# Optimization experiments

Hardware: AMD Instinct MI355X
Metric: run time of the kernel (lower is better)

The kernel has to match this reference:

```python
import jax, jax.numpy as jnp
import numpy as np

B, S, D = 4, 2048, 512
H, DH = 8, 64  # head_num, atten_dim
EPS = 1e-5


def setup_inputs() -> dict:
    key = jax.random.key(0)
    ks = jax.random.split(key, 24)
    sc_in = 1.0 / np.sqrt(D)
    sc_hid = 1.0 / np.sqrt(H * DH)
    inp = {}
    names = ["Q_data", "Q_time", "K_data", "K_time", "V_data", "V_time"]
    for i, n in enumerate(names):
        inp[n] = jax.random.normal(ks[i], (B, S, D), dtype=jnp.float32)
    # projection weights stored as [in, out]
    pnames = ["q_d", "q_t", "k_d", "k_t", "v_d", "v_t"]
    for i, p in enumerate(pnames):
        inp["W" + p] = jax.random.normal(ks[6 + 2 * i], (D, H * DH), dtype=jnp.float32) * sc_in
        inp["b" + p] = jax.random.normal(ks[7 + 2 * i], (H * DH,), dtype=jnp.float32) * 0.01
    inp["Wo"] = jax.random.normal(ks[18], (H * DH, D), dtype=jnp.float32) * sc_hid
    inp["bo"] = jax.random.normal(ks[19], (D,), dtype=jnp.float32) * 0.01
    inp["gamma"] = jnp.ones((D,), dtype=jnp.float32)
    inp["beta"] = jnp.zeros((D,), dtype=jnp.float32)
    return inp


def _proj(x, W, b):
    # [B,S,D] @ [D,H*DH] -> [B,S,H,DH]
    return (jnp.einsum('bsd,de->bse', x, W) + b).reshape(B, S, H, DH)


def reference(Q_data, Q_time, K_data, K_time, V_data, V_time,
              Wq_d, bq_d, Wq_t, bq_t, Wk_d, bk_d, Wk_t, bk_t,
              Wv_d, bv_d, Wv_t, bv_t, Wo, bo, gamma, beta):
    residual = Q_data
    qd = _proj(Q_data, Wq_d, bq_d)
    qt = _proj(Q_time, Wq_t, bq_t)
    kd = _proj(K_data, Wk_d, bk_d)
    kt = _proj(K_time, Wk_t, bk_t)
    vd = _proj(V_data, Wv_d, bv_d)
    vt = _proj(V_time, Wv_t, bv_t)
    scale = 1.0 / np.sqrt(DH)
    # combined dual-stream scores: [B,H,S,S]
    scores = (jnp.einsum('bshd,bthd->bhst', qd, kd)
              + jnp.einsum('bshd,bthd->bhst', qt, kt)) * scale
    attn = jax.nn.softmax(scores, axis=-1)
    # dual V context, summed: [B,S,H,DH]
    ctx = jnp.einsum('bhst,bthd->bshd', attn, vd + vt)
    ctx = ctx.reshape(B, S, H * DH)
    out = jnp.einsum('bse,ed->bsd', ctx, Wo) + bo
    x = out + residual
    mu = jnp.mean(x, axis=-1, keepdims=True)
    var = jnp.var(x, axis=-1, keepdims=True)
    return (x - mu) * jax.lax.rsqrt(var + EPS) * gamma + beta
```

## Files before the change

### kernel.cpp

```cpp
#include <hip/hip_runtime.h>
#include <hip/hip_bf16.h>

#define DEVI __device__ __forceinline__

typedef __attribute__((ext_vector_type(4))) float f32x4;
typedef __attribute__((ext_vector_type(8))) short s16x8;
typedef __bf16 bf16x8 __attribute__((ext_vector_type(8)));

static constexpr int B_ = 4, S_ = 2048, D_ = 512, H_ = 8;
static constexpr int BS = B_ * S_;
static constexpr float QSCALE = 0.125f * 1.4426950408889634f;

DEVI unsigned short f2bf(float x) {
  union { float f; unsigned int u; } v; v.f = x;
  unsigned int r = v.u + 0x7FFFu + ((v.u >> 16) & 1u);
  return (unsigned short)(r >> 16);
}

DEVI void gload16(const void* g, void* l) {
  __builtin_amdgcn_global_load_lds(
      (const __attribute__((address_space(1))) unsigned int*)g,
      (__attribute__((address_space(3))) unsigned int*)l, 16, 0, 0);
}

DEVI f32x4 mfma16(s16x8 a, s16x8 b, f32x4 c) {
  return __builtin_amdgcn_mfma_f32_16x16x32_bf16(
      __builtin_bit_cast(bf16x8, a), __builtin_bit_cast(bf16x8, b), c, 0, 0, 0);
}

__global__ void k_cvt_x(const float* __restrict__ x0, const float* __restrict__ x1,
                        const float* __restrict__ x2, const float* __restrict__ x3,
                        const float* __restrict__ x4, const float* __restrict__ x5,
                        unsigned short* __restrict__ xc) {
  const int p = blockIdx.y;
  const float* x = (p == 0) ? x0 : (p == 1) ? x1 : (p == 2) ? x2
                 : (p == 3) ? x3 : (p == 4) ? x4 : x5;
  const int i = (blockIdx.x * 256 + threadIdx.x) * 4;
  const float4 v = *(const float4*)(x + i);
  ushort4 o;
  o.x = f2bf(v.x); o.y = f2bf(v.y); o.z = f2bf(v.z); o.w = f2bf(v.w);
  *(ushort4*)(xc + (size_t)p * BS * D_ + i) = o;
}

__global__ void k_cvt_w(const float* __restrict__ w0, const float* __restrict__ w1,
                        const float* __restrict__ w2, const float* __restrict__ w3,
                        const float* __restrict__ w4, const float* __restrict__ w5,
                        const float* __restrict__ w6, unsigned short* __restrict__ wt) {
  const int p = blockIdx.y;
  const float* w = (p == 0) ? w0 : (p == 1) ? w1 : (p == 2) ? w2
                 : (p == 3) ? w3 : (p == 4) ? w4 : (p == 5) ? w5 : w6;
  __shared__ float t[32][33];
  const int tx = threadIdx.x, ty = threadIdx.y;
  const int tn = (blockIdx.x & 15) * 32, tk = (blockIdx.x >> 4) * 32;
#pragma unroll
  for (int i = 0; i < 4; ++i)
    t[ty + i * 8][tx] = w[(size_t)(tk + ty + i * 8) * 512 + tn + tx];
  __syncthreads();
#pragma unroll
  for (int i = 0; i < 4; ++i)
    wt[(size_t)p * 262144 + (size_t)(tn + ty + i * 8) * 512 + tk + tx] =
        f2bf(t[tx][ty + i * 8]);
}

__launch_bounds__(256, 2)
__global__ void k_proj(const unsigned short* __restrict__ Xc, const unsigned short* __restrict__ Wt,
                       const float* __restrict__ b0, const float* __restrict__ b1,
                       const float* __restrict__ b2, const float* __restrict__ b3,
                       const float* __restrict__ b4, const float* __restrict__ b5,
                       unsigned short* __restrict__ Qc, unsigned short* __restrict__ Kc,
                       unsigned short* __restrict__ Vt) {
  __shared__ unsigned short As[128 * 32], Bs[128 * 32];
  const int p = blockIdx.y;
  const int m0 = (blockIdx.x >> 2) * 128, n0 = (blockIdx.x & 3) * 128;
  const int tid = threadIdx.x, w = tid >> 6, lane = tid & 63;
  const int g = lane >> 4, cl = lane & 15;
  const int wm = (w >> 1) * 64, wn = (w & 1) * 64;
  f32x4 acc[4][4];
#pragma unroll
  for (int i = 0; i < 4; ++i)
#pragma unroll
    for (int j = 0; j < 4; ++j) { acc[i][j][0] = 0.f; acc[i][j][1] = 0.f; acc[i][j][2] = 0.f; acc[i][j][3] = 0.f; }

  const int npass = (p == 4) ? 2 : 1;
  for (int pass = 0; pass < npass; ++pass) {
    const int src = (p == 4) ? (4 + pass) : p;
    const unsigned short* A = Xc + (size_t)src * BS * 512;
    const unsigned short* Bw = Wt + (size_t)src * 262144;
    for (int k0 = 0; k0 < 512; k0 += 32) {
#pragma unroll
      for (int i = 0; i < 2; ++i) {
        const int c = i * 256 + tid;
        gload16(A + (size_t)(m0 + (c >> 2)) * 512 + k0 + (c & 3) * 8,
                (char*)As + (i * 256 + w * 64) * 16);
        gload16(Bw + (size_t)(n0 + (c >> 2)) * 512 + k0 + (c & 3) * 8,
                (char*)Bs + (i * 256 + w * 64) * 16);
      }
      __syncthreads();
      s16x8 af[4], bf[4];
#pragma unroll
      for (int t = 0; t < 4; ++t) {
        af[t] = *(const s16x8*)(As + (wm + t * 16 + cl) * 32 + g * 8);
        bf[t] = *(const s16x8*)(Bs + (wn + t * 16 + cl) * 32 + g * 8);
      }
#pragma unroll
      for (int mt = 0; mt < 4; ++mt)
#pragma unroll
        for (int nt = 0; nt < 4; ++nt)
          acc[mt][nt] = mfma16(af[mt], bf[nt], acc[mt][nt]);
      __syncthreads();
    }
  }
  const float scale = (p <= 1) ? QSCALE : 1.0f;
#pragma unroll
  for (int nt = 0; nt < 4; ++nt) {
    const int n = n0 + wn + nt * 16 + cl;
    float bias;
    if (p == 0) bias = b0[n]; else if (p == 1) bias = b1[n];
    else if (p == 2) bias = b2[n]; else if (p == 3) bias = b3[n];
    else bias = b4[n] + b5[n];
    const int h = n >> 6, dh = n & 63;
    if (p == 4) {
#pragma unroll
      for (int mt = 0; mt < 4; ++mt) {
        const int m = m0 + wm + mt * 16 + g * 4;
        const int bb = m >> 11, s = m & 2047;
        ushort4 o4;
        o4.x = f2bf(acc[mt][nt][0] + bias);
        o4.y = f2bf(acc[mt][nt][1] + bias);
        o4.z = f2bf(acc[mt][nt][2] + bias);
        o4.w = f2bf(acc[mt][nt][3] + bias);
        *(ushort4*)(&Vt[((size_t)(bb * 8 + h) * 64 + dh) * 2048 + s]) = o4;
      }
    } else {
#pragma unroll
      for (int mt = 0; mt < 4; ++mt)
#pragma unroll
        for (int r = 0; r < 4; ++r) {
          const int m = m0 + wm + mt * 16 + g * 4 + r;
          const int bb = m >> 11, s = m & 2047;
          const unsigned short o = f2bf((acc[mt][nt][r] + bias) * scale);
          if (p <= 1) {
            Qc[(((size_t)(bb * 8 + h) * 2048 + s) << 7) + dh + p * 64] = o;
          } else {
            const int dk = dh + (p - 2) * 64;
            Kc[(((size_t)(bb * 8 + h) * 2048 + s) << 7) + (dk ^ ((s & 7) << 3))] = o;
          }
        }
    }
  }
}

__launch_bounds__(256, 1)
__global__ void k_attn(const unsigned short* __restrict__ Qc, const unsigned short* __restrict__ Kc,
                       const unsigned short* __restrict__ Vt, unsigned short* __restrict__ Cx) {
  __shared__ unsigned short Ks[2][64 * 128];
  __shared__ unsigned short Ps[4][64 * 88];
  const int bid = blockIdx.x;
  const int xcd = bid & 7, idx = bid >> 3;
  const int bh = xcd | ((idx & 3) << 3);
  const int qblk = idx >> 2;
  const int tid = threadIdx.x, w = tid >> 6, lane = tid & 63;
  const int g = lane >> 4, cl = lane & 15;
  const unsigned short* Qb = Qc + (size_t)bh * S_ * 128;
  const unsigned short* Kb = Kc + (size_t)bh * S_ * 128;
  const unsigned short* Vb = Vt + (size_t)bh * 64 * S_;
  const int q0 = qblk * 256 + w * 64;

  s16x8 qf[4][4];
#pragma unroll
  for (int qb = 0; qb < 4; ++qb)
#pragma unroll
    for (int ks = 0; ks < 4; ++ks)
      qf[qb][ks] = *(const s16x8*)(Qb + (size_t)(q0 + qb * 16 + cl) * 128 + ks * 32 + g * 8);

  const f32x4 z4 = {0.f, 0.f, 0.f, 0.f};
  f32x4 ctx[4][5];
#pragma unroll
  for (int qb = 0; qb < 4; ++qb)
#pragma unroll
    for (int nt = 0; nt < 5; ++nt) ctx[qb][nt] = z4;

  const unsigned short* vrow[4];
#pragma unroll
  for (int nt = 0; nt < 4; ++nt) vrow[nt] = Vb + (size_t)(nt * 16 + cl) * 2048 + g * 8;

  const unsigned short* kptr[4];
#pragma unroll
  for (int i = 0; i < 4; ++i)
    kptr[i] = Kb + (size_t)((w * 4 + i) * 4 + (lane >> 4)) * 128 + (lane & 15) * 8;

  const short onev = (cl == 0) ? (short)0x3F80 : (short)0;
  const s16x8 vfo = {onev, onev, onev, onev, onev, onev, onev, onev};

  unsigned short* Pw = Ps[w];

#pragma unroll
  for (int i = 0; i < 4; ++i) {
    gload16(kptr[i], (char*)Ks[0] + (w * 4 + i) * 1024);
    kptr[i] += 64 * 128;
  }
  __syncthreads();

  const int NT = S_ / 64;
  for (int t = 0; t < NT; ++t) {
    const int b = t & 1;
    if (t + 1 < NT) {
#pragma unroll
      for (int i = 0; i < 4; ++i) {
        gload16(kptr[i], (char*)Ks[b ^ 1] + (w * 4 + i) * 1024);
        kptr[i] += 64 * 128;
      }
    }
    s16x8 vreg[2][4];
#pragma unroll
    for (int kk = 0; kk < 2; ++kk)
#pragma unroll
      for (int nt = 0; nt < 4; ++nt)
        vreg[kk][nt] = *(const s16x8*)(vrow[nt] + t * 64 + kk * 32);

#pragma unroll
    for (int kb = 0; kb < 4; ++kb) {
      f32x4 sq[4];
#pragma unroll
      for (int qb = 0; qb < 4; ++qb) sq[qb] = z4;
#pragma unroll
      for (int ks = 0; ks < 4; ++ks) {
        const s16x8 kf = *(const s16x8*)((const char*)Ks[b] + (kb * 16 + cl) * 256 +
                                         ((ks * 64 + g * 16) ^ ((cl & 7) << 4)));
        sq[0] = mfma16(kf, qf[0][ks], sq[0]);
        sq[1] = mfma16(kf, qf[1][ks], sq[1]);
        sq[2] = mfma16(kf, qf[2][ks], sq[2]);
        sq[3] = mfma16(kf, qf[3][ks], sq[3]);
      }
#pragma unroll
      for (int qb = 0; qb < 4; ++qb) {
        const float e0 = exp2f(sq[qb][0]);
        const float e1 = exp2f(sq[qb][1]);
        const float e2 = exp2f(sq[qb][2]);
        const float e3 = exp2f(sq[qb][3]);
        unsigned int p01, p23;
        asm("v_cvt_pk_bf16_f32 %0, %1, %2" : "=v"(p01) : "v"(e0), "v"(e1));
        asm("v_cvt_pk_bf16_f32 %0, %1, %2" : "=v"(p23) : "v"(e2), "v"(e3));
        uint2 pk; pk.x = p01; pk.y = p23;
        *(uint2*)((char*)Pw + (qb * 16 + cl) * 176 + kb * 32 + g * 8) = pk;
      }
    }

    s16x8 pa[4][2];
#pragma unroll
    for (int qb = 0; qb < 4; ++qb)
#pragma unroll
      for (int kk = 0; kk < 2; ++kk)
        pa[qb][kk] = *(const s16x8*)((const char*)Pw + (qb * 16 + cl) * 176 + kk * 64 + g * 16);
#pragma unroll
    for (int kk = 0; kk < 2; ++kk) {
#pragma unroll
      for (int nt = 0; nt < 4; ++nt) {
        ctx[0][nt] = mfma16(pa[0][kk], vreg[kk][nt], ctx[0][nt]);
        ctx[1][nt] = mfma16(pa[1][kk], vreg[kk][nt], ctx[1][nt]);
        ctx[2][nt] = mfma16(pa[2][kk], vreg[kk][nt], ctx[2][nt]);
        ctx[3][nt] = mfma16(pa[3][kk], vreg[kk][nt], ctx[3][nt]);
      }
#pragma unroll
      for (int qb = 0; qb < 4; ++qb)
        ctx[qb][4] = mfma16(pa[qb][kk], vfo, ctx[qb][4]);
    }
    __syncthreads();
  }

  const int bb = bh >> 3, h = bh & 7;
#pragma unroll
  for (int qb = 0; qb < 4; ++qb) {
    float inv[4];
#pragma unroll
    for (int r = 0; r < 4; ++r)
      inv[r] = 1.0f / __shfl(ctx[qb][4][r], lane & 48);
#pragma unroll
    for (int nt = 0; nt < 4; ++nt)
#pragma unroll
      for (int r = 0; r < 4; ++r) {
        const int s = q0 + qb * 16 + g * 4 + r;
        Cx[(size_t)(bb * 2048 + s) * 512 + h * 64 + nt * 16 + cl] =
            f2bf(ctx[qb][nt][r] * inv[r]);
      }
  }
}

__launch_bounds__(256, 2)
__global__ void k_oproj(const unsigned short* __restrict__ Cx, const unsigned short* __restrict__ Wo,
                        const float* __restrict__ bo, const float* __restrict__ resid,
                        float* __restrict__ tmp) {
  __shared__ unsigned short As[128 * 32], Bs[128 * 32];
  const int m0 = (blockIdx.x >> 2) * 128, n0 = (blockIdx.x & 3) * 128;
  const int tid = threadIdx.x, w = tid >> 6, lane = tid & 63;
  const int g = lane >> 4, cl = lane & 15;
  const int wm = (w >> 1) * 64, wn = (w & 1) * 64;
  f32x4 acc[4][4];
#pragma unroll
  for (int i = 0; i < 4; ++i)
#pragma unroll
    for (int j = 0; j < 4; ++j) { acc[i][j][0] = 0.f; acc[i][j][1] = 0.f; acc[i][j][2] = 0.f; acc[i][j][3] = 0.f; }
  for (int k0 = 0; k0 < 512; k0 += 32) {
#pragma unroll
    for (int i = 0; i < 2; ++i) {
      const int c = i * 256 + tid;
      gload16(Cx + (size_t)(m0 + (c >> 2)) * 512 + k0 + (c & 3) * 8,
              (char*)As + (i * 256 + w * 64) * 16);
      gload16(Wo + (size_t)(n0 + (c >> 2)) * 512 + k0 + (c & 3) * 8,
              (char*)Bs + (i * 256 + w * 64) * 16);
    }
    __syncthreads();
    s16x8 af[4], bf[4];
#pragma unroll
    for (int t = 0; t < 4; ++t) {
      af[t] = *(const s16x8*)(As + (wm + t * 16 + cl) * 32 + g * 8);
      bf[t] = *(const s16x8*)(Bs + (wn + t * 16 + cl) * 32 + g * 8);
    }
#pragma unroll
    for (int mt = 0; mt < 4; ++mt)
#pragma unroll
      for (int nt = 0; nt < 4; ++nt)
        acc[mt][nt] = mfma16(af[mt], bf[nt], acc[mt][nt]);
    __syncthreads();
  }
#pragma unroll
  for (int nt = 0; nt < 4; ++nt) {
    const int n = n0 + wn + nt * 16 + cl;
    const float bias = bo[n];
#pragma unroll
    for (int mt = 0; mt < 4; ++mt)
#pragma unroll
      for (int r = 0; r < 4; ++r) {
        const int m = m0 + wm + mt * 16 + g * 4 + r;
        tmp[(size_t)m * 512 + n] = acc[mt][nt][r] + bias + resid[(size_t)m * 512 + n];
      }
  }
}

__global__ void k_ln(const float* __restrict__ tmp, const float* __restrict__ gamma,
                     const float* __restrict__ beta, float* __restrict__ out) {
  const int row = blockIdx.x * 4 + (threadIdx.x >> 6);
  const int lane = threadIdx.x & 63;
  const float* x = tmp + (size_t)row * 512 + lane * 8;
  const float4 a = *(const float4*)x;
  const float4 c = *(const float4*)(x + 4);
  float s = a.x + a.y + a.z + a.w + c.x + c.y + c.z + c.w;
  float s2 = a.x * a.x + a.y * a.y + a.z * a.z + a.w * a.w +
             c.x * c.x + c.y * c.y + c.z * c.z + c.w * c.w;
#pragma unroll
  for (int off = 1; off < 64; off <<= 1) { s += __shfl_xor(s, off); s2 += __shfl_xor(s2, off); }
  const float mu = s * (1.0f / 512.0f);
  const float var = s2 * (1.0f / 512.0f) - mu * mu;
  const float rstd = rsqrtf(var + 1e-5f);
  const float4 g0 = *(const float4*)(gamma + lane * 8);
  const float4 g1 = *(const float4*)(gamma + lane * 8 + 4);
  const float4 b0 = *(const float4*)(beta + lane * 8);
  const float4 b1 = *(const float4*)(beta + lane * 8 + 4);
  float4 o0, o1;
  o0.x = (a.x - mu) * rstd * g0.x + b0.x; o0.y = (a.y - mu) * rstd * g0.y + b0.y;
  o0.z = (a.z - mu) * rstd * g0.z + b0.z; o0.w = (a.w - mu) * rstd * g0.w + b0.w;
  o1.x = (c.x - mu) * rstd * g1.x + b1.x; o1.y = (c.y - mu) * rstd * g1.y + b1.y;
  o1.z = (c.z - mu) * rstd * g1.z + b1.z; o1.w = (c.w - mu) * rstd * g1.w + b1.w;
  *(float4*)(out + (size_t)row * 512 + lane * 8) = o0;
  *(float4*)(out + (size_t)row * 512 + lane * 8 + 4) = o1;
}

extern "C" void kernel_launch(void* const* d_in, const int* in_sizes, int n_in,
                              void* d_out, int out_size, void* d_ws, size_t ws_size,
                              hipStream_t stream) {
  const float* Qd = (const float*)d_in[0];
  const float* Qt = (const float*)d_in[1];
  const float* Kd = (const float*)d_in[2];
  const float* Kt = (const float*)d_in[3];
  const float* Vd = (const float*)d_in[4];
  const float* Vtm = (const float*)d_in[5];
  const float* Wqd = (const float*)d_in[6];  const float* bqd = (const float*)d_in[7];
  const float* Wqt = (const float*)d_in[8];  const float* bqt = (const float*)d_in[9];
  const float* Wkd = (const float*)d_in[10]; const float* bkd = (const float*)d_in[11];
  const float* Wkt = (const float*)d_in[12]; const float* bkt = (const float*)d_in[13];
  const float* Wvd = (const float*)d_in[14]; const float* bvd = (const float*)d_in[15];
  const float* Wvt = (const float*)d_in[16]; const float* bvt = (const float*)d_in[17];
  const float* Wo  = (const float*)d_in[18]; const float* bo  = (const float*)d_in[19];
  const float* gamma = (const float*)d_in[20];
  const float* beta  = (const float*)d_in[21];

  char* ws = (char*)d_ws;
  size_t off = 0;
  auto alloc = [&](size_t bytes) { void* p = ws + off; off += (bytes + 255) & ~(size_t)255; return p; };
  unsigned short* Xc = (unsigned short*)alloc((size_t)6 * BS * 512 * 2);
  unsigned short* Wt = (unsigned short*)alloc((size_t)7 * 512 * 512 * 2);
  unsigned short* Qc = (unsigned short*)alloc((size_t)B_ * H_ * S_ * 128 * 2);
  unsigned short* Kc = (unsigned short*)alloc((size_t)B_ * H_ * S_ * 128 * 2);
  unsigned short* Vt = (unsigned short*)alloc((size_t)B_ * H_ * 64 * S_ * 2);
  unsigned short* Cx = (unsigned short*)Xc;
  float* tmp = (float*)((char*)Xc + (size_t)BS * 512 * 2);

  k_cvt_x<<<dim3(BS * D_ / 4 / 256, 6), 256, 0, stream>>>(Qd, Qt, Kd, Kt, Vd, Vtm, Xc);
  k_cvt_w<<<dim3(256, 7), dim3(32, 8), 0, stream>>>(Wqd, Wqt, Wkd, Wkt, Wvd, Wvt, Wo, Wt);
  k_proj<<<dim3(256, 5), 256, 0, stream>>>(Xc, Wt, bqd, bqt, bkd, bkt, bvd, bvt, Qc, Kc, Vt);
  k_attn<<<dim3(256), 256, 0, stream>>>(Qc, Kc, Vt, Cx);
  k_oproj<<<dim3(256), 256, 0, stream>>>(Cx, Wt + (size_t)6 * 262144, bo, Qd, tmp);
  k_ln<<<dim3(BS / 4), 256, 0, stream>>>(tmp, gamma, beta, (float*)d_out);
}
```

Measured before the change: 372.3 us.

## Halve attention query tile per block and launch twice as many blocks

The attention kernel now gives each wave 32 query rows instead of 64, so a block covers 128 queries and the grid grows from 256 to 512 blocks. Launch bounds move to two blocks per CU, and the block-to-(head, query-block) mapping is reordered so that all query blocks of a head land on the same XCD. The aim is better CU occupancy and latency hiding on a GPU with 256 CUs. In exchange, every key/value tile is loaded and reused across half as many queries, which doubles K/V traffic per unit of work.

```diff
diff --git a/kernel.cpp b/kernel.cpp
--- a/kernel.cpp
+++ b/kernel.cpp
@@ -150,33 +150,32 @@
   }
 }
 
-__launch_bounds__(256, 1)
+__launch_bounds__(256, 2)
 __global__ void k_attn(const unsigned short* __restrict__ Qc, const unsigned short* __restrict__ Kc,
                        const unsigned short* __restrict__ Vt, unsigned short* __restrict__ Cx) {
   __shared__ unsigned short Ks[2][64 * 128];
-  __shared__ unsigned short Ps[4][64 * 88];
+  __shared__ unsigned short Ps[4][32 * 88];
   const int bid = blockIdx.x;
-  const int xcd = bid & 7, idx = bid >> 3;
-  const int bh = xcd | ((idx & 3) << 3);
-  const int qblk = idx >> 2;
+  const int orig = (bid & 7) * 64 + (bid >> 3);
+  const int bh = orig >> 4, qblk = orig & 15;
   const int tid = threadIdx.x, w = tid >> 6, lane = tid & 63;
   const int g = lane >> 4, cl = lane & 15;
   const unsigned short* Qb = Qc + (size_t)bh * S_ * 128;
   const unsigned short* Kb = Kc + (size_t)bh * S_ * 128;
   const unsigned short* Vb = Vt + (size_t)bh * 64 * S_;
-  const int q0 = qblk * 256 + w * 64;
-
-  s16x8 qf[4][4];
-#pragma unroll
-  for (int qb = 0; qb < 4; ++qb)
+  const int q0 = qblk * 128 + w * 32;
+
+  s16x8 qf[2][4];
+#pragma unroll
+  for (int qb = 0; qb < 2; ++qb)
 #pragma unroll
     for (int ks = 0; ks < 4; ++ks)
       qf[qb][ks] = *(const s16x8*)(Qb + (size_t)(q0 + qb * 16 + cl) * 128 + ks * 32 + g * 8);
 
   const f32x4 z4 = {0.f, 0.f, 0.f, 0.f};
-  f32x4 ctx[4][5];
-#pragma unroll
-  for (int qb = 0; qb < 4; ++qb)
+  f32x4 ctx[2][5];
+#pragma unroll
+  for (int qb = 0; qb < 2; ++qb)
 #pragma unroll
     for (int nt = 0; nt < 5; ++nt) ctx[qb][nt] = z4;
 
@@ -184,10 +183,8 @@
 #pragma unroll
   for (int nt = 0; nt < 4; ++nt) vrow[nt] = Vb + (size_t)(nt * 16 + cl) * 2048 + g * 8;
 
-  const unsigned short* kptr[4];
-#pragma unroll
-  for (int i = 0; i < 4; ++i)
-    kptr[i] = Kb + (size_t)((w * 4 + i) * 4 + (lane >> 4)) * 128 + (lane & 15) * 8;
+  const unsigned short* kptr =
+      Kb + (size_t)((w * 4) * 4 + (lane >> 4)) * 128 + (lane & 15) * 8;
 
   const short onev = (cl == 0) ? (short)0x3F80 : (short)0;
   const s16x8 vfo = {onev, onev, onev, onev, onev, onev, onev, onev};
@@ -195,10 +192,9 @@
   unsigned short* Pw = Ps[w];
 
 #pragma unroll
-  for (int i = 0; i < 4; ++i) {
-    gload16(kptr[i], (char*)Ks[0] + (w * 4 + i) * 1024);
-    kptr[i] += 64 * 128;
-  }
+  for (int i = 0; i < 4; ++i)
+    gload16(kptr + i * 512, (char*)Ks[0] + (w * 4 + i) * 1024);
+  kptr += 64 * 128;
   __syncthreads();
 
   const int NT = S_ / 64;
@@ -206,10 +202,9 @@
     const int b = t & 1;
     if (t + 1 < NT) {
 #pragma unroll
-      for (int i = 0; i < 4; ++i) {
-        gload16(kptr[i], (char*)Ks[b ^ 1] + (w * 4 + i) * 1024);
-        kptr[i] += 64 * 128;
-      }
+      for (int i = 0; i < 4; ++i)
+        gload16(kptr + i * 512, (char*)Ks[b ^ 1] + (w * 4 + i) * 1024);
+      kptr += 64 * 128;
     }
     s16x8 vreg[2][4];
 #pragma unroll
@@ -220,20 +215,17 @@
 
 #pragma unroll
     for (int kb = 0; kb < 4; ++kb) {
-      f32x4 sq[4];
-#pragma unroll
-      for (int qb = 0; qb < 4; ++qb) sq[qb] = z4;
+      f32x4 sq[2];
+      sq[0] = z4; sq[1] = z4;
 #pragma unroll
       for (int ks = 0; ks < 4; ++ks) {
         const s16x8 kf = *(const s16x8*)((const char*)Ks[b] + (kb * 16 + cl) * 256 +
                                          ((ks * 64 + g * 16) ^ ((cl & 7) << 4)));
         sq[0] = mfma16(kf, qf[0][ks], sq[0]);
         sq[1] = mfma16(kf, qf[1][ks], sq[1]);
-        sq[2] = mfma16(kf, qf[2][ks], sq[2]);
-        sq[3] = mfma16(kf, qf[3][ks], sq[3]);
-      }
-#pragma unroll
-      for (int qb = 0; qb < 4; ++qb) {
+      }
+#pragma unroll
+      for (int qb = 0; qb < 2; ++qb) {
         const float e0 = exp2f(sq[qb][0]);
         const float e1 = exp2f(sq[qb][1]);
         const float e2 = exp2f(sq[qb][2]);
@@ -246,9 +238,9 @@
       }
     }
 
-    s16x8 pa[4][2];
-#pragma unroll
-    for (int qb = 0; qb < 4; ++qb)
+    s16x8 pa[2][2];
+#pragma unroll
+    for (int qb = 0; qb < 2; ++qb)
 #pragma unroll
       for (int kk = 0; kk < 2; ++kk)
         pa[qb][kk] = *(const s16x8*)((const char*)Pw + (qb * 16 + cl) * 176 + kk * 64 + g * 16);
@@ -258,19 +250,16 @@
       for (int nt = 0; nt < 4; ++nt) {
         ctx[0][nt] = mfma16(pa[0][kk], vreg[kk][nt], ctx[0][nt]);
         ctx[1][nt] = mfma16(pa[1][kk], vreg[kk][nt], ctx[1][nt]);
-        ctx[2][nt] = mfma16(pa[2][kk], vreg[kk][nt], ctx[2][nt]);
-        ctx[3][nt] = mfma16(pa[3][kk], vreg[kk][nt], ctx[3][nt]);
-      }
-#pragma unroll
-      for (int qb = 0; qb < 4; ++qb)
-        ctx[qb][4] = mfma16(pa[qb][kk], vfo, ctx[qb][4]);
+      }
+      ctx[0][4] = mfma16(pa[0][kk], vfo, ctx[0][4]);
+      ctx[1][4] = mfma16(pa[1][kk], vfo, ctx[1][4]);
     }
     __syncthreads();
   }
 
   const int bb = bh >> 3, h = bh & 7;
 #pragma unroll
-  for (int qb = 0; qb < 4; ++qb) {
+  for (int qb = 0; qb < 2; ++qb) {
     float inv[4];
 #pragma unroll
     for (int r = 0; r < 4; ++r)
@@ -398,7 +387,7 @@
   k_cvt_x<<<dim3(BS * D_ / 4 / 256, 6), 256, 0, stream>>>(Qd, Qt, Kd, Kt, Vd, Vtm, Xc);
   k_cvt_w<<<dim3(256, 7), dim3(32, 8), 0, stream>>>(Wqd, Wqt, Wkd, Wkt, Wvd, Wvt, Wo, Wt);
   k_proj<<<dim3(256, 5), 256, 0, stream>>>(Xc, Wt, bqd, bqt, bkd, bkt, bvd, bvt, Qc, Kc, Vt);
-  k_attn<<<dim3(256), 256, 0, stream>>>(Qc, Kc, Vt, Cx);
+  k_attn<<<dim3(512), 256, 0, stream>>>(Qc, Kc, Vt, Cx);
   k_oproj<<<dim3(256), 256, 0, stream>>>(Cx, Wt + (size_t)6 * 262144, bo, Qd, tmp);
   k_ln<<<dim3(BS / 4), 256, 0, stream>>>(tmp, gamma, beta, (float*)d_out);
 }
```

New measurement: 350.0 us. 1.06x faster.
